# Performance work log

Measured on AMD Instinct MI355X. Metric: run time of the kernel, lower is better.

Reference implementation:

```python
import jax, jax.numpy as jnp
import numpy as np

DIM = 512
HEADS = 8
HD = DIM // HEADS

def _rotate_half(t):
    t1, t2 = jnp.split(t, 2, axis=-1)
    return jnp.concatenate((-t2, t1), axis=-1)

def _layernorm(x, g, b, eps=1e-5):
    mu = jnp.mean(x, axis=-1, keepdims=True)
    var = jnp.var(x, axis=-1, keepdims=True)
    return (x - mu) * jax.lax.rsqrt(var + eps) * g + b

def setup_inputs() -> dict:
    key = jax.random.key(0)
    ks = jax.random.split(key, 12)
    B, S = 4, 2048
    x = jax.random.normal(ks[0], (B, S, DIM), dtype=jnp.float32)
    rope_cos = jax.random.uniform(ks[1], (1, S, 1, HD), dtype=jnp.float32)
    rope_sin = jax.random.uniform(ks[2], (1, S, 1, HD), dtype=jnp.float32)
    sd = 1.0 / np.sqrt(DIM)
    params = {
        'norm1_g': jnp.ones((DIM,), jnp.float32),
        'norm1_b': jnp.zeros((DIM,), jnp.float32),
        'norm2_g': jnp.ones((DIM,), jnp.float32),
        'norm2_b': jnp.zeros((DIM,), jnp.float32),
        'w_qkv': jax.random.uniform(ks[3], (DIM, 3 * DIM), jnp.float32, -sd, sd),
        'b_qkv': jax.random.uniform(ks[4], (3 * DIM,), jnp.float32, -sd, sd),
        'w_proj': jax.random.uniform(ks[5], (DIM, DIM), jnp.float32, -sd, sd),
        'b_proj': jax.random.uniform(ks[6], (DIM,), jnp.float32, -sd, sd),
        'w_fc1': jax.random.uniform(ks[7], (DIM, 4 * DIM), jnp.float32, -sd, sd),
        'b_fc1': jax.random.uniform(ks[8], (4 * DIM,), jnp.float32, -sd, sd),
        'w_fc2': jax.random.uniform(ks[9], (4 * DIM, DIM), jnp.float32, -1.0 / np.sqrt(4 * DIM), 1.0 / np.sqrt(4 * DIM)),
        'b_fc2': jax.random.uniform(ks[10], (DIM,), jnp.float32, -1.0 / np.sqrt(4 * DIM), 1.0 / np.sqrt(4 * DIM)),
    }
    return {'x': x, 'rope_cos': rope_cos, 'rope_sin': rope_sin, **params}

def reference(x, rope_cos, rope_sin, norm1_g, norm1_b, norm2_g, norm2_b,
              w_qkv, b_qkv, w_proj, b_proj, w_fc1, b_fc1, w_fc2, b_fc2):
    B, S, D = x.shape
    scale = 1.0 / np.sqrt(HD)
    shortcut = x
    h = _layernorm(x, norm1_g, norm1_b)
    qkv = (h @ w_qkv + b_qkv).reshape(B, S, 3, HEADS, HD)
    q, k, v = qkv[:, :, 0], qkv[:, :, 1], qkv[:, :, 2]  # [B,S,H,hd]
    q = q * rope_cos + _rotate_half(q) * rope_sin
    k = k * rope_cos + _rotate_half(k) * rope_sin
    # attention over heads: scores [B,H,S,S]
    attn = jnp.einsum('bqhd,bkhd->bhqk', q, k) * scale
    attn = jax.nn.softmax(attn, axis=-1)
    o = jnp.einsum('bhqk,bkhd->bqhd', attn, v).reshape(B, S, D)
    o = o @ w_proj + b_proj
    x = shortcut + o  # dropout is identity in eval
    h2 = _layernorm(x, norm2_g, norm2_b)
    mlp = jax.nn.gelu(h2 @ w_fc1 + b_fc1, approximate=False) @ w_fc2 + b_fc2
    return x + mlp
```

## Files before the change

### kernel.cpp

```cpp
#include <hip/hip_runtime.h>
#include <cstdint>
#include <cstddef>

typedef unsigned short u16;
typedef unsigned int   u32;
typedef __bf16 bf16x8 __attribute__((ext_vector_type(8)));
typedef float  f32x4  __attribute__((ext_vector_type(4)));
typedef u16    u16x4  __attribute__((ext_vector_type(4)));

#define BS   8192
#define DIMM 512
#define NH   8
#define HD   64
#define SEQ  2048
#define DFF  2048
#define NQKV 1536

#define GLD16(g, l) __builtin_amdgcn_global_load_lds( \
    (__attribute__((address_space(1))) const void*)(g), \
    (__attribute__((address_space(3))) void*)(l), 16, 0, 0)

__device__ __forceinline__ float b2f(u16 s) {
  u32 u = ((u32)s) << 16;
  float f; __builtin_memcpy(&f, &u, 4); return f;
}
__device__ __forceinline__ u16 f2b(float f) {
  u32 u; __builtin_memcpy(&u, &f, 4);
  u += 0x7fffu + ((u >> 16) & 1u);
  return (u16)(u >> 16);
}

__global__ __launch_bounds__(256) void transpose_k(const float* __restrict__ W,
                                                   u16* __restrict__ WT, int Kd, int Nd) {
  int idx = blockIdx.x * 256 + threadIdx.x;
  if (idx < Kd * Nd) {
    int n = idx / Kd, k = idx - n * Kd;
    WT[idx] = f2b(W[(size_t)k * Nd + n]);
  }
}

__global__ __launch_bounds__(256) void ln_f32b_k(const float* __restrict__ X,
    const float* __restrict__ G, const float* __restrict__ Bb, u16* __restrict__ out) {
  int w = threadIdx.x >> 6, lane = threadIdx.x & 63;
  size_t row = (size_t)blockIdx.x * 4 + w;
  const float* xr = X + row * DIMM;
  float v[8];
  *(float4*)&v[0] = *(const float4*)(xr + lane * 8);
  *(float4*)&v[4] = *(const float4*)(xr + lane * 8 + 4);
  float s = 0.f, s2 = 0.f;
#pragma unroll
  for (int j = 0; j < 8; j++) { s += v[j]; s2 += v[j] * v[j]; }
#pragma unroll
  for (int m = 1; m < 64; m <<= 1) { s += __shfl_xor(s, m); s2 += __shfl_xor(s2, m); }
  float mu = s * (1.f / DIMM);
  float rsd = rsqrtf(s2 * (1.f / DIMM) - mu * mu + 1e-5f);
  float g[8], bb[8];
  *(float4*)&g[0]  = *(const float4*)(G + lane * 8);
  *(float4*)&g[4]  = *(const float4*)(G + lane * 8 + 4);
  *(float4*)&bb[0] = *(const float4*)(Bb + lane * 8);
  *(float4*)&bb[4] = *(const float4*)(Bb + lane * 8 + 4);
  uint4 ov; u16* os = (u16*)&ov;
#pragma unroll
  for (int j = 0; j < 8; j++) os[j] = f2b((v[j] - mu) * rsd * g[j] + bb[j]);
  *(uint4*)(out + row * DIMM + lane * 8) = ov;
}

template <int EPI>
__global__ __launch_bounds__(256) void gemm_bt(const u16* __restrict__ A,
    const u16* __restrict__ BT, const float* __restrict__ bias,
    void* __restrict__ Cout, const float* __restrict__ resid, int N, int Kd) {
  __shared__ u16 a_s[128 * 32];
  __shared__ u16 b_s[128 * 32];
  int t = threadIdx.x, lane = t & 63, w = t >> 6;
  int l15 = lane & 15, quad = lane >> 4;
  int m0 = blockIdx.y * 128, n0 = blockIdx.x * 128;
  int wm = (w >> 1) * 64, wn = (w & 1) * 64;
  f32x4 z4 = {0.f, 0.f, 0.f, 0.f};
  f32x4 acc[4][4];
#pragma unroll
  for (int i = 0; i < 4; i++)
#pragma unroll
    for (int j = 0; j < 4; j++) acc[i][j] = z4;

  for (int k0 = 0; k0 < Kd; k0 += 32) {
    __syncthreads();
#pragma unroll
    for (int i = 0; i < 2; i++) {
      int c = t + i * 256;
      int row = c >> 2, ch = c & 3;
      GLD16(A  + (size_t)(m0 + row) * Kd + k0 + ch * 8, &a_s[c * 8]);
      GLD16(BT + (size_t)(n0 + row) * Kd + k0 + ch * 8, &b_s[c * 8]);
    }
    __syncthreads();
    bf16x8 af[4], bfm[4];
#pragma unroll
    for (int mt = 0; mt < 4; mt++) af[mt]  = *(const bf16x8*)&a_s[(wm + mt * 16 + l15) * 32 + quad * 8];
#pragma unroll
    for (int nt = 0; nt < 4; nt++) bfm[nt] = *(const bf16x8*)&b_s[(wn + nt * 16 + l15) * 32 + quad * 8];
#pragma unroll
    for (int mt = 0; mt < 4; mt++)
#pragma unroll
      for (int nt = 0; nt < 4; nt++)
        acc[mt][nt] = __builtin_amdgcn_mfma_f32_16x16x32_bf16(af[mt], bfm[nt], acc[mt][nt], 0, 0, 0);
  }

#pragma unroll
  for (int nt = 0; nt < 4; nt++) {
    int col = n0 + wn + nt * 16 + l15;
    float bv = bias[col];
#pragma unroll
    for (int mt = 0; mt < 4; mt++) {
#pragma unroll
      for (int r = 0; r < 4; r++) {
        int rw = m0 + wm + mt * 16 + quad * 4 + r;
        float v = acc[mt][nt][r] + bv;
        size_t off = (size_t)rw * N + col;
        if (EPI == 0) {
          ((float*)Cout)[off] = v;
        } else if (EPI == 1) {
          ((float*)Cout)[off] = v + resid[off];
        } else {
          ((u16*)Cout)[off] = f2b(0.5f * v * (1.f + erff(v * 0.70710678118654752f)));
        }
      }
    }
  }
}

__global__ __launch_bounds__(256) void rope_k(const float* __restrict__ qkv,
    const float* __restrict__ C, const float* __restrict__ Sn,
    u16* __restrict__ Qo, u16* __restrict__ Ko, u16* __restrict__ Vo) {
  int idx = blockIdx.x * 256 + threadIdx.x;
  int row = idx / 384;
  int cn = idx - row * 384;
  int n0 = cn * 4;
  int comp = n0 >> 9;
  int hh = (n0 >> 6) & 7;
  int d0 = n0 & 63;
  int b = row >> 11, s = row & 2047;
  const float* src = qkv + (size_t)row * NQKV;
  float4 val = *(const float4*)(src + n0);
  float* vs = (float*)&val;
  size_t oo = ((size_t)((b << 3) + hh) * SEQ + s) * HD + d0;
  if (comp == 2) {
    u16x4 ov;
#pragma unroll
    for (int j = 0; j < 4; j++) ov[j] = f2b(vs[j]);
    *(u16x4*)(Vo + oo) = ov;
    return;
  }
  float4 pv = *(const float4*)(src + (n0 ^ 32));
  float4 cv = *(const float4*)(C + s * HD + d0);
  float4 sv = *(const float4*)(Sn + s * HD + d0);
  float *ps = (float*)&pv, *cs = (float*)&cv, *ss = (float*)&sv;
  float sgn = (d0 & 32) ? 1.f : -1.f;
  float sc = (comp == 0) ? 0.125f : 1.f;
  u16x4 ov;
#pragma unroll
  for (int j = 0; j < 4; j++)
    ov[j] = f2b(sc * (vs[j] * cs[j] + sgn * ps[j] * ss[j]));
  *(u16x4*)((comp == 0 ? Qo : Ko) + oo) = ov;
}

__global__ __launch_bounds__(256) void attn_flash_k(const u16* __restrict__ Qg,
    const u16* __restrict__ Kg, const u16* __restrict__ Vg, u16* __restrict__ Og) {
  __shared__ u16 q_s[64 * 72];
  __shared__ u16 k_s[64 * 72];
  __shared__ u16 vt_s[64 * 72];
  int t = threadIdx.x, lane = t & 63, w = t >> 6;
  int l15 = lane & 15, quad = lane >> 4;
  int bh = blockIdx.x >> 5;
  int qt0 = (blockIdx.x & 31) * 64;
  int b = bh >> 3, h = bh & 7;
  const u16* Qp = Qg + (size_t)bh * SEQ * HD;
  const u16* Kp = Kg + (size_t)bh * SEQ * HD;
  const u16* Vp = Vg + (size_t)bh * SEQ * HD;
  int row0 = t >> 3, ch = t & 7;
  int row1 = row0 + 32;
  int r8a = row0 >> 3, r0a = row0 & 7;
  int r8b = row1 >> 3, r0b = row1 & 7;

  *(uint4*)&q_s[row0 * 72 + ch * 8] = *(const uint4*)(Qp + (size_t)(qt0 + row0) * HD + ch * 8);
  *(uint4*)&q_s[row1 * 72 + ch * 8] = *(const uint4*)(Qp + (size_t)(qt0 + row1) * HD + ch * 8);
  uint4 kr0 = *(const uint4*)(Kp + (size_t)row0 * HD + ch * 8);
  uint4 kr1 = *(const uint4*)(Kp + (size_t)row1 * HD + ch * 8);
  uint4 vr0 = *(const uint4*)(Vp + (size_t)row0 * HD + ch * 8);
  uint4 vr1 = *(const uint4*)(Vp + (size_t)row1 * HD + ch * 8);
  __syncthreads();
  bf16x8 qa[2];
  qa[0] = *(const bf16x8*)&q_s[(w * 16 + l15) * 72 + quad * 8];
  qa[1] = *(const bf16x8*)&q_s[(w * 16 + l15) * 72 + 32 + quad * 8];
  u16* p_s = q_s;
  f32x4 z4 = {0.f, 0.f, 0.f, 0.f};
  f32x4 of[4];
#pragma unroll
  for (int n = 0; n < 4; n++) of[n] = z4;
  float lrun[4] = {0.f, 0.f, 0.f, 0.f};

  for (int kt = 0; kt < SEQ; kt += 64) {
    __syncthreads();
    *(uint4*)&k_s[row0 * 72 + ch * 8] = kr0;
    *(uint4*)&k_s[row1 * 72 + ch * 8] = kr1;
    {
      u16* v0 = (u16*)&vr0; u16* v1 = (u16*)&vr1;
#pragma unroll
      for (int j = 0; j < 8; j++) {
        int d = ch * 8 + j;
        vt_s[d * 72 + ((r8a ^ ch) << 3) + r0a] = v0[j];
        vt_s[d * 72 + ((r8b ^ ch) << 3) + r0b] = v1[j];
      }
    }
    __syncthreads();
    if (kt + 64 < SEQ) {
      kr0 = *(const uint4*)(Kp + (size_t)(kt + 64 + row0) * HD + ch * 8);
      kr1 = *(const uint4*)(Kp + (size_t)(kt + 64 + row1) * HD + ch * 8);
      vr0 = *(const uint4*)(Vp + (size_t)(kt + 64 + row0) * HD + ch * 8);
      vr1 = *(const uint4*)(Vp + (size_t)(kt + 64 + row1) * HD + ch * 8);
    }
    f32x4 sf[4];
#pragma unroll
    for (int n = 0; n < 4; n++) sf[n] = z4;
#pragma unroll
    for (int kk = 0; kk < 2; kk++)
#pragma unroll
      for (int n = 0; n < 4; n++) {
        bf16x8 kb = *(const bf16x8*)&k_s[(n * 16 + l15) * 72 + kk * 32 + quad * 8];
        sf[n] = __builtin_amdgcn_mfma_f32_16x16x32_bf16(qa[kk], kb, sf[n], 0, 0, 0);
      }
    float pw[4][4];
#pragma unroll
    for (int r = 0; r < 4; r++)
#pragma unroll
      for (int n = 0; n < 4; n++) {
        float pp = __expf(sf[n][r]);
        pw[r][n] = pp;
        lrun[r] += pp;
      }
#pragma unroll
    for (int r = 0; r < 4; r++)
#pragma unroll
      for (int n = 0; n < 4; n++)
        p_s[w * 1152 + (quad * 4 + r) * 72 + n * 16 + l15] = f2b(pw[r][n]);
#pragma unroll
    for (int kk = 0; kk < 2; kk++) {
      bf16x8 pa = *(const bf16x8*)&p_s[w * 1152 + l15 * 72 + kk * 32 + quad * 8];
#pragma unroll
      for (int n = 0; n < 4; n++) {
        bf16x8 vb = *(const bf16x8*)&vt_s[(n * 16 + l15) * 72 +
                     (((kk * 4 + quad) ^ (2 * n + (l15 >> 3))) << 3)];
        of[n] = __builtin_amdgcn_mfma_f32_16x16x32_bf16(pa, vb, of[n], 0, 0, 0);
      }
    }
  }
#pragma unroll
  for (int r = 0; r < 4; r++) {
    float l = lrun[r];
#pragma unroll
    for (int m = 1; m < 16; m <<= 1) l += __shfl_xor(l, m);
    float inv = 1.f / l;
    size_t orow = (size_t)(b * SEQ + qt0 + w * 16 + quad * 4 + r);
#pragma unroll
    for (int n = 0; n < 4; n++)
      Og[orow * DIMM + h * HD + n * 16 + l15] = f2b(of[n][r] * inv);
  }
}

extern "C" void kernel_launch(void* const* d_in, const int* in_sizes, int n_in,
                              void* d_out, int out_size, void* d_ws, size_t ws_size,
                              hipStream_t stream) {
  const float* x    = (const float*)d_in[0];
  const float* rc   = (const float*)d_in[1];
  const float* rsn  = (const float*)d_in[2];
  const float* n1g  = (const float*)d_in[3];
  const float* n1b  = (const float*)d_in[4];
  const float* n2g  = (const float*)d_in[5];
  const float* n2b  = (const float*)d_in[6];
  const float* wqkv = (const float*)d_in[7];
  const float* bqkv = (const float*)d_in[8];
  const float* wprj = (const float*)d_in[9];
  const float* bprj = (const float*)d_in[10];
  const float* wf1  = (const float*)d_in[11];
  const float* bf1  = (const float*)d_in[12];
  const float* wf2  = (const float*)d_in[13];
  const float* bf2  = (const float*)d_in[14];

  char* p = (char*)d_ws;
  u16*   wqkvT = (u16*)p;
  u16*   wprjT = (u16*)(p + (2u  << 20));
  u16*   wf1T  = (u16*)(p + (3u  << 20));
  u16*   wf2T  = (u16*)(p + (5u  << 20));
  u16*   h1    = (u16*)(p + (8u  << 20));
  float* qkvb  = (float*)(p + (16u << 20));
  u16*   Qb    = (u16*)(p + (64u << 20));
  u16*   Kb    = (u16*)(p + (72u << 20));
  u16*   Vb    = (u16*)(p + (80u << 20));
  float* x2    = (float*)(p + (88u << 20));
  u16*   ob    = h1;
  u16*   h2    = h1;
  u16*   mid   = (u16*)qkvb;

  transpose_k<<<dim3((DIMM * NQKV + 255) / 256), 256, 0, stream>>>(wqkv, wqkvT, DIMM, NQKV);
  transpose_k<<<dim3((DIMM * DIMM + 255) / 256), 256, 0, stream>>>(wprj, wprjT, DIMM, DIMM);
  transpose_k<<<dim3((DIMM * DFF  + 255) / 256), 256, 0, stream>>>(wf1,  wf1T,  DIMM, DFF);
  transpose_k<<<dim3((DFF  * DIMM + 255) / 256), 256, 0, stream>>>(wf2,  wf2T,  DFF,  DIMM);

  ln_f32b_k<<<dim3(BS / 4), 256, 0, stream>>>(x, n1g, n1b, h1);

  gemm_bt<0><<<dim3(NQKV / 128, BS / 128), 256, 0, stream>>>(h1, wqkvT, bqkv, qkvb, nullptr, NQKV, DIMM);

  rope_k<<<dim3(BS * NQKV / 4 / 256), 256, 0, stream>>>(qkvb, rc, rsn, Qb, Kb, Vb);

  attn_flash_k<<<dim3(32 * (SEQ / 64)), 256, 0, stream>>>(Qb, Kb, Vb, ob);

  gemm_bt<1><<<dim3(DIMM / 128, BS / 128), 256, 0, stream>>>(ob, wprjT, bprj, x2, x, DIMM, DIMM);

  ln_f32b_k<<<dim3(BS / 4), 256, 0, stream>>>(x2, n2g, n2b, h2);

  gemm_bt<2><<<dim3(DFF / 128, BS / 128), 256, 0, stream>>>(h2, wf1T, bf1, mid, nullptr, DFF, DIMM);

  gemm_bt<1><<<dim3(DIMM / 128, BS / 128), 256, 0, stream>>>(mid, wf2T, bf2, (float*)d_out, x2, DIMM, DFF);
}
```

Measured before the change: 346.5 us.

## Fuse weight transposes, emit bf16 QKV, widen rope, and double query tile in attention

Merges the four weight-transpose launches into one kernel. The QKV GEMM now writes bf16 instead of fp32, which halves that intermediate's traffic, and rope reads and writes 8 elements per thread. The attention kernel processes 128 queries per block so each K/V tile is reused twice. It folds log2(e) into the Q scale to use exp2f and truncates P to bf16 instead of rounding. The costs are extra rounding error in qkv and P, and half as many attention blocks for occupancy.

```diff
diff --git a/kernel.cpp b/kernel.cpp
--- a/kernel.cpp
+++ b/kernel.cpp
@@ -6,7 +6,6 @@
 typedef unsigned int   u32;
 typedef __bf16 bf16x8 __attribute__((ext_vector_type(8)));
 typedef float  f32x4  __attribute__((ext_vector_type(4)));
-typedef u16    u16x4  __attribute__((ext_vector_type(4)));
 
 #define BS   8192
 #define DIMM 512
@@ -29,14 +28,28 @@
   u += 0x7fffu + ((u >> 16) & 1u);
   return (u16)(u >> 16);
 }
-
-__global__ __launch_bounds__(256) void transpose_k(const float* __restrict__ W,
-                                                   u16* __restrict__ WT, int Kd, int Nd) {
+__device__ __forceinline__ u16 f2b_rtz(float f) {
+  u32 u; __builtin_memcpy(&u, &f, 4);
+  return (u16)(u >> 16);
+}
+
+#define SZ_QKV (DIMM * NQKV)
+#define SZ_PRJ (DIMM * DIMM)
+#define SZ_F1  (DIMM * DFF)
+#define SZ_F2  (DFF * DIMM)
+__global__ __launch_bounds__(256) void transpose_all_k(
+    const float* __restrict__ w_qkv, const float* __restrict__ w_prj,
+    const float* __restrict__ w_f1,  const float* __restrict__ w_f2,
+    u16* __restrict__ o_qkv, u16* __restrict__ o_prj,
+    u16* __restrict__ o_f1,  u16* __restrict__ o_f2) {
   int idx = blockIdx.x * 256 + threadIdx.x;
-  if (idx < Kd * Nd) {
-    int n = idx / Kd, k = idx - n * Kd;
-    WT[idx] = f2b(W[(size_t)k * Nd + n]);
-  }
+  const float* W; u16* O; int Kd, Nd, off;
+  if (idx < SZ_QKV)                         { W = w_qkv; O = o_qkv; Kd = DIMM; Nd = NQKV; off = idx; }
+  else if (idx < SZ_QKV + SZ_PRJ)           { W = w_prj; O = o_prj; Kd = DIMM; Nd = DIMM; off = idx - SZ_QKV; }
+  else if (idx < SZ_QKV + SZ_PRJ + SZ_F1)   { W = w_f1;  O = o_f1;  Kd = DIMM; Nd = DFF;  off = idx - SZ_QKV - SZ_PRJ; }
+  else                                      { W = w_f2;  O = o_f2;  Kd = DFF;  Nd = DIMM; off = idx - SZ_QKV - SZ_PRJ - SZ_F1; }
+  int n = off / Kd, k = off - n * Kd;
+  O[off] = f2b(W[(size_t)k * Nd + n]);
 }
 
 __global__ __launch_bounds__(256) void ln_f32b_k(const float* __restrict__ X,
@@ -119,58 +132,58 @@
           ((float*)Cout)[off] = v;
         } else if (EPI == 1) {
           ((float*)Cout)[off] = v + resid[off];
+        } else if (EPI == 2) {
+          ((u16*)Cout)[off] = f2b(0.5f * v * (1.f + erff(v * 0.70710678118654752f)));
         } else {
-          ((u16*)Cout)[off] = f2b(0.5f * v * (1.f + erff(v * 0.70710678118654752f)));
+          ((u16*)Cout)[off] = f2b(v);
         }
       }
     }
   }
 }
 
-__global__ __launch_bounds__(256) void rope_k(const float* __restrict__ qkv,
+#define QSCALE 0.18033688f
+__global__ __launch_bounds__(256) void rope_k(const u16* __restrict__ qkv,
     const float* __restrict__ C, const float* __restrict__ Sn,
     u16* __restrict__ Qo, u16* __restrict__ Ko, u16* __restrict__ Vo) {
   int idx = blockIdx.x * 256 + threadIdx.x;
-  int row = idx / 384;
-  int cn = idx - row * 384;
-  int n0 = cn * 4;
+  int row = idx / 192;
+  int cn = idx - row * 192;
+  int n0 = cn * 8;
   int comp = n0 >> 9;
   int hh = (n0 >> 6) & 7;
   int d0 = n0 & 63;
   int b = row >> 11, s = row & 2047;
-  const float* src = qkv + (size_t)row * NQKV;
-  float4 val = *(const float4*)(src + n0);
-  float* vs = (float*)&val;
+  const u16* src = qkv + (size_t)row * NQKV;
+  uint4 val = *(const uint4*)(src + n0);
+  u16* vs = (u16*)&val;
   size_t oo = ((size_t)((b << 3) + hh) * SEQ + s) * HD + d0;
-  if (comp == 2) {
-    u16x4 ov;
-#pragma unroll
-    for (int j = 0; j < 4; j++) ov[j] = f2b(vs[j]);
-    *(u16x4*)(Vo + oo) = ov;
-    return;
-  }
-  float4 pv = *(const float4*)(src + (n0 ^ 32));
-  float4 cv = *(const float4*)(C + s * HD + d0);
-  float4 sv = *(const float4*)(Sn + s * HD + d0);
-  float *ps = (float*)&pv, *cs = (float*)&cv, *ss = (float*)&sv;
+  if (comp == 2) { *(uint4*)(Vo + oo) = val; return; }
+  uint4 pv = *(const uint4*)(src + (n0 ^ 32));
+  u16* ps = (u16*)&pv;
+  float cv[8], sv[8];
+  *(float4*)&cv[0] = *(const float4*)(C + s * HD + d0);
+  *(float4*)&cv[4] = *(const float4*)(C + s * HD + d0 + 4);
+  *(float4*)&sv[0] = *(const float4*)(Sn + s * HD + d0);
+  *(float4*)&sv[4] = *(const float4*)(Sn + s * HD + d0 + 4);
   float sgn = (d0 & 32) ? 1.f : -1.f;
-  float sc = (comp == 0) ? 0.125f : 1.f;
-  u16x4 ov;
-#pragma unroll
-  for (int j = 0; j < 4; j++)
-    ov[j] = f2b(sc * (vs[j] * cs[j] + sgn * ps[j] * ss[j]));
-  *(u16x4*)((comp == 0 ? Qo : Ko) + oo) = ov;
+  float sc = (comp == 0) ? QSCALE : 1.f;
+  uint4 ov; u16* os = (u16*)&ov;
+#pragma unroll
+  for (int j = 0; j < 8; j++)
+    os[j] = f2b(sc * (b2f(vs[j]) * cv[j] + sgn * b2f(ps[j]) * sv[j]));
+  *(uint4*)((comp == 0 ? Qo : Ko) + oo) = ov;
 }
 
 __global__ __launch_bounds__(256) void attn_flash_k(const u16* __restrict__ Qg,
     const u16* __restrict__ Kg, const u16* __restrict__ Vg, u16* __restrict__ Og) {
-  __shared__ u16 q_s[64 * 72];
+  __shared__ u16 q_s[128 * 72];
   __shared__ u16 k_s[64 * 72];
   __shared__ u16 vt_s[64 * 72];
   int t = threadIdx.x, lane = t & 63, w = t >> 6;
   int l15 = lane & 15, quad = lane >> 4;
-  int bh = blockIdx.x >> 5;
-  int qt0 = (blockIdx.x & 31) * 64;
+  int bh = blockIdx.x >> 4;
+  int qt0 = (blockIdx.x & 15) * 128;
   int b = bh >> 3, h = bh & 7;
   const u16* Qp = Qg + (size_t)bh * SEQ * HD;
   const u16* Kp = Kg + (size_t)bh * SEQ * HD;
@@ -180,22 +193,30 @@
   int r8a = row0 >> 3, r0a = row0 & 7;
   int r8b = row1 >> 3, r0b = row1 & 7;
 
-  *(uint4*)&q_s[row0 * 72 + ch * 8] = *(const uint4*)(Qp + (size_t)(qt0 + row0) * HD + ch * 8);
-  *(uint4*)&q_s[row1 * 72 + ch * 8] = *(const uint4*)(Qp + (size_t)(qt0 + row1) * HD + ch * 8);
+#pragma unroll
+  for (int i = 0; i < 4; i++) {
+    int c = t + i * 256, qr = c >> 3, qc = c & 7;
+    *(uint4*)&q_s[qr * 72 + qc * 8] = *(const uint4*)(Qp + (size_t)(qt0 + qr) * HD + qc * 8);
+  }
   uint4 kr0 = *(const uint4*)(Kp + (size_t)row0 * HD + ch * 8);
   uint4 kr1 = *(const uint4*)(Kp + (size_t)row1 * HD + ch * 8);
   uint4 vr0 = *(const uint4*)(Vp + (size_t)row0 * HD + ch * 8);
   uint4 vr1 = *(const uint4*)(Vp + (size_t)row1 * HD + ch * 8);
   __syncthreads();
-  bf16x8 qa[2];
-  qa[0] = *(const bf16x8*)&q_s[(w * 16 + l15) * 72 + quad * 8];
-  qa[1] = *(const bf16x8*)&q_s[(w * 16 + l15) * 72 + 32 + quad * 8];
+  bf16x8 qa[2][2];
+#pragma unroll
+  for (int rs = 0; rs < 2; rs++) {
+    qa[rs][0] = *(const bf16x8*)&q_s[(rs * 64 + w * 16 + l15) * 72 + quad * 8];
+    qa[rs][1] = *(const bf16x8*)&q_s[(rs * 64 + w * 16 + l15) * 72 + 32 + quad * 8];
+  }
   u16* p_s = q_s;
   f32x4 z4 = {0.f, 0.f, 0.f, 0.f};
-  f32x4 of[4];
-#pragma unroll
-  for (int n = 0; n < 4; n++) of[n] = z4;
-  float lrun[4] = {0.f, 0.f, 0.f, 0.f};
+  f32x4 of[2][4];
+#pragma unroll
+  for (int rs = 0; rs < 2; rs++)
+#pragma unroll
+    for (int n = 0; n < 4; n++) of[rs][n] = z4;
+  float lrun[2][4] = {};
 
   for (int kt = 0; kt < SEQ; kt += 64) {
     __syncthreads();
@@ -217,52 +238,57 @@
       vr0 = *(const uint4*)(Vp + (size_t)(kt + 64 + row0) * HD + ch * 8);
       vr1 = *(const uint4*)(Vp + (size_t)(kt + 64 + row1) * HD + ch * 8);
     }
-    f32x4 sf[4];
-#pragma unroll
-    for (int n = 0; n < 4; n++) sf[n] = z4;
+    f32x4 sf[2][4];
+#pragma unroll
+    for (int rs = 0; rs < 2; rs++)
+#pragma unroll
+      for (int n = 0; n < 4; n++) sf[rs][n] = z4;
 #pragma unroll
     for (int kk = 0; kk < 2; kk++)
 #pragma unroll
       for (int n = 0; n < 4; n++) {
         bf16x8 kb = *(const bf16x8*)&k_s[(n * 16 + l15) * 72 + kk * 32 + quad * 8];
-        sf[n] = __builtin_amdgcn_mfma_f32_16x16x32_bf16(qa[kk], kb, sf[n], 0, 0, 0);
-      }
-    float pw[4][4];
-#pragma unroll
-    for (int r = 0; r < 4; r++)
-#pragma unroll
-      for (int n = 0; n < 4; n++) {
-        float pp = __expf(sf[n][r]);
-        pw[r][n] = pp;
-        lrun[r] += pp;
-      }
-#pragma unroll
-    for (int r = 0; r < 4; r++)
-#pragma unroll
-      for (int n = 0; n < 4; n++)
-        p_s[w * 1152 + (quad * 4 + r) * 72 + n * 16 + l15] = f2b(pw[r][n]);
+        sf[0][n] = __builtin_amdgcn_mfma_f32_16x16x32_bf16(qa[0][kk], kb, sf[0][n], 0, 0, 0);
+        sf[1][n] = __builtin_amdgcn_mfma_f32_16x16x32_bf16(qa[1][kk], kb, sf[1][n], 0, 0, 0);
+      }
+#pragma unroll
+    for (int rs = 0; rs < 2; rs++)
+#pragma unroll
+      for (int r = 0; r < 4; r++) {
+        int prow = (rs * 64 + w * 16 + quad * 4 + r) * 72;
+#pragma unroll
+        for (int n = 0; n < 4; n++) {
+          float pp = exp2f(sf[rs][n][r]);
+          lrun[rs][r] += pp;
+          p_s[prow + n * 16 + l15] = f2b_rtz(pp);
+        }
+      }
 #pragma unroll
     for (int kk = 0; kk < 2; kk++) {
-      bf16x8 pa = *(const bf16x8*)&p_s[w * 1152 + l15 * 72 + kk * 32 + quad * 8];
+      bf16x8 pa0 = *(const bf16x8*)&p_s[(w * 16 + l15) * 72 + kk * 32 + quad * 8];
+      bf16x8 pa1 = *(const bf16x8*)&p_s[(64 + w * 16 + l15) * 72 + kk * 32 + quad * 8];
 #pragma unroll
       for (int n = 0; n < 4; n++) {
         bf16x8 vb = *(const bf16x8*)&vt_s[(n * 16 + l15) * 72 +
                      (((kk * 4 + quad) ^ (2 * n + (l15 >> 3))) << 3)];
-        of[n] = __builtin_amdgcn_mfma_f32_16x16x32_bf16(pa, vb, of[n], 0, 0, 0);
-      }
-    }
-  }
-#pragma unroll
-  for (int r = 0; r < 4; r++) {
-    float l = lrun[r];
-#pragma unroll
-    for (int m = 1; m < 16; m <<= 1) l += __shfl_xor(l, m);
-    float inv = 1.f / l;
-    size_t orow = (size_t)(b * SEQ + qt0 + w * 16 + quad * 4 + r);
-#pragma unroll
-    for (int n = 0; n < 4; n++)
-      Og[orow * DIMM + h * HD + n * 16 + l15] = f2b(of[n][r] * inv);
-  }
+        of[0][n] = __builtin_amdgcn_mfma_f32_16x16x32_bf16(pa0, vb, of[0][n], 0, 0, 0);
+        of[1][n] = __builtin_amdgcn_mfma_f32_16x16x32_bf16(pa1, vb, of[1][n], 0, 0, 0);
+      }
+    }
+  }
+#pragma unroll
+  for (int rs = 0; rs < 2; rs++)
+#pragma unroll
+    for (int r = 0; r < 4; r++) {
+      float l = lrun[rs][r];
+#pragma unroll
+      for (int m = 1; m < 16; m <<= 1) l += __shfl_xor(l, m);
+      float inv = 1.f / l;
+      size_t orow = (size_t)(b * SEQ + qt0 + rs * 64 + w * 16 + quad * 4 + r);
+#pragma unroll
+      for (int n = 0; n < 4; n++)
+        Og[orow * DIMM + h * HD + n * 16 + l15] = f2b(of[rs][n][r] * inv);
+    }
 }
 
 extern "C" void kernel_launch(void* const* d_in, const int* in_sizes, int n_in,
@@ -290,27 +316,25 @@
   u16*   wf1T  = (u16*)(p + (3u  << 20));
   u16*   wf2T  = (u16*)(p + (5u  << 20));
   u16*   h1    = (u16*)(p + (8u  << 20));
-  float* qkvb  = (float*)(p + (16u << 20));
+  u16*   qkvb  = (u16*)(p + (16u << 20));
   u16*   Qb    = (u16*)(p + (64u << 20));
   u16*   Kb    = (u16*)(p + (72u << 20));
   u16*   Vb    = (u16*)(p + (80u << 20));
   float* x2    = (float*)(p + (88u << 20));
   u16*   ob    = h1;
   u16*   h2    = h1;
-  u16*   mid   = (u16*)qkvb;
-
-  transpose_k<<<dim3((DIMM * NQKV + 255) / 256), 256, 0, stream>>>(wqkv, wqkvT, DIMM, NQKV);
-  transpose_k<<<dim3((DIMM * DIMM + 255) / 256), 256, 0, stream>>>(wprj, wprjT, DIMM, DIMM);
-  transpose_k<<<dim3((DIMM * DFF  + 255) / 256), 256, 0, stream>>>(wf1,  wf1T,  DIMM, DFF);
-  transpose_k<<<dim3((DFF  * DIMM + 255) / 256), 256, 0, stream>>>(wf2,  wf2T,  DFF,  DIMM);
+  u16*   mid   = qkvb;
+
+  transpose_all_k<<<dim3((SZ_QKV + SZ_PRJ + SZ_F1 + SZ_F2) / 256), 256, 0, stream>>>(
+      wqkv, wprj, wf1, wf2, wqkvT, wprjT, wf1T, wf2T);
 
   ln_f32b_k<<<dim3(BS / 4), 256, 0, stream>>>(x, n1g, n1b, h1);
 
-  gemm_bt<0><<<dim3(NQKV / 128, BS / 128), 256, 0, stream>>>(h1, wqkvT, bqkv, qkvb, nullptr, NQKV, DIMM);
-
-  rope_k<<<dim3(BS * NQKV / 4 / 256), 256, 0, stream>>>(qkvb, rc, rsn, Qb, Kb, Vb);
-
-  attn_flash_k<<<dim3(32 * (SEQ / 64)), 256, 0, stream>>>(Qb, Kb, Vb, ob);
+  gemm_bt<3><<<dim3(NQKV / 128, BS / 128), 256, 0, stream>>>(h1, wqkvT, bqkv, qkvb, nullptr, NQKV, DIMM);
+
+  rope_k<<<dim3(BS * NQKV / 8 / 256), 256, 0, stream>>>(qkvb, rc, rsn, Qb, Kb, Vb);
+
+  attn_flash_k<<<dim3(32 * (SEQ / 128)), 256, 0, stream>>>(Qb, Kb, Vb, ob);
 
   gemm_bt<1><<<dim3(DIMM / 128, BS / 128), 256, 0, stream>>>(ob, wprjT, bprj, x2, x, DIMM, DIMM);
 
```

Measured after the change: 331.5 us. 4.3% less time.
